# Optimization experiments

Measured on AMD Instinct MI355X. Metric: run time of the kernel, lower is better.

The kernel has to match this reference:

```python
import jax, jax.numpy as jnp
import numpy as np

N = 100000      # nodes
E = 1600000     # edges (before self loops)
H = 64          # hidden channels (per-head out dim, concat=False)
HEADS = 2
L = 2           # num GAT blocks
IN = 64
OUT = 10
B = 64          # graphs in batch
SLOPE = 0.2     # LeakyReLU negative slope (GATv2Conv default)
EPS = 1e-5      # BatchNorm eps


def setup_inputs() -> dict:
    key = jax.random.key(0)
    ks = jax.random.split(key, 10)
    s = 0.05
    x = jax.random.normal(ks[0], (N, IN), jnp.float32)
    edge_index = jax.random.randint(ks[1], (2, E), 0, N, dtype=jnp.int64)
    batch = jnp.sort(jax.random.randint(ks[2], (N,), 0, B, dtype=jnp.int64))
    W_enc = jax.random.normal(ks[3], (IN, H), jnp.float32) * s
    b_enc = jnp.zeros((H,), jnp.float32)
    Wl = jax.random.normal(ks[4], (L, H, HEADS * H), jnp.float32) * s
    bl = jnp.zeros((L, HEADS * H), jnp.float32)
    Wr = jax.random.normal(ks[5], (L, H, HEADS * H), jnp.float32) * s
    br = jnp.zeros((L, HEADS * H), jnp.float32)
    att = jax.random.normal(ks[6], (L, HEADS, H), jnp.float32) * s
    bias = jnp.zeros((L, H), jnp.float32)
    gamma = jnp.ones((L, H), jnp.float32)
    beta = jnp.zeros((L, H), jnp.float32)
    W_cls = jax.random.normal(ks[7], (H, OUT), jnp.float32) * s
    b_cls = jnp.zeros((OUT,), jnp.float32)
    return dict(x=x, edge_index=edge_index, batch=batch, W_enc=W_enc, b_enc=b_enc,
                Wl=Wl, bl=bl, Wr=Wr, br=br, att=att, bias=bias,
                gamma=gamma, beta=beta, W_cls=W_cls, b_cls=b_cls)


def reference(x, edge_index, batch, W_enc, b_enc, Wl, bl, Wr, br, att, bias,
              gamma, beta, W_cls, b_cls):
    # add self loops (GATv2Conv default add_self_loops=True)
    loops = jnp.arange(N, dtype=edge_index.dtype)
    ei = jnp.concatenate([edge_index, jnp.stack([loops, loops])], axis=1)
    src, dst = ei[0], ei[1]

    h = x @ W_enc + b_enc                                   # [N, H] atom encoder (Linear)
    for l in range(L):
        xl = (h @ Wl[l] + bl[l]).reshape(N, HEADS, H)       # source transform
        xr = (h @ Wr[l] + br[l]).reshape(N, HEADS, H)       # target transform
        # GATv2: e_uv = a^T LeakyReLU(W_l x_u + W_r x_v)
        z = jax.nn.leaky_relu(xl[src] + xr[dst], SLOPE)     # [E', heads, H]
        e = jnp.einsum('ehc,hc->eh', z, att[l])             # [E', heads]
        # segment softmax over incoming edges of each dst node
        m = jax.ops.segment_max(e, dst, num_segments=N)     # [N, heads]
        ex = jnp.exp(e - m[dst])
        den = jax.ops.segment_sum(ex, dst, num_segments=N)
        alpha = ex / den[dst]                               # [E', heads]
        out = jax.ops.segment_sum(xl[src] * alpha[:, :, None], dst, num_segments=N)
        h_new = out.mean(axis=1) + bias[l]                  # concat=False: mean over heads
        # BatchNorm1d (batch statistics) -> ReLU; dropout=0
        mu = h_new.mean(axis=0)
        var = h_new.var(axis=0)
        h = jax.nn.relu((h_new - mu) * jax.lax.rsqrt(var + EPS) * gamma[l] + beta[l])

    # global mean pool over graphs
    cnt = jax.ops.segment_sum(jnp.ones((N,), h.dtype), batch, num_segments=B)
    g = jax.ops.segment_sum(h, batch, num_segments=B) / jnp.maximum(cnt, 1.0)[:, None]
    return g @ W_cls + b_cls                                # [B, OUT]
```

## Files before the change

kernel.cpp:

```cpp
#include <hip/hip_runtime.h>

#define N_NODES 100000
#define E_EDGES 1600000
#define EP_EDGES (E_EDGES + N_NODES)
#define SLOPE 0.2f
#define BN_EPS 1e-5f
#define NB 8
#define NODES_PER_B 12500
#define NREP 32
#define SUBREG 8192
#define SCATTER_BLKS ((EP_EDGES + 255) / 256)

typedef _Float16 h2 __attribute__((ext_vector_type(2)));

#if defined(__has_builtin)
#if __has_builtin(__builtin_amdgcn_fdot2)
#define HAVE_FDOT2 1
#endif
#endif

__device__ __forceinline__ float fdot2f(h2 a, h2 b, float c) {
#ifdef HAVE_FDOT2
    return __builtin_amdgcn_fdot2(a, b, c, false);
#else
    return c + (float)a[0] * (float)b[0] + (float)a[1] * (float)b[1];
#endif
}
__device__ __forceinline__ h2 bch2(unsigned u) { return __builtin_bit_cast(h2, u); }
__device__ __forceinline__ h2 habs2(h2 z) {
    return __builtin_bit_cast(h2, (unsigned)(__builtin_bit_cast(unsigned, z) & 0x7fff7fffu));
}
__device__ __forceinline__ h2 shflx_h2(h2 a, int o) {
    return __builtin_bit_cast(h2, __shfl_xor(__builtin_bit_cast(int, a), o, 64));
}

template <int CTRL>
__device__ __forceinline__ float dpp_add_step(float v) {
    int r = __builtin_amdgcn_update_dpp(0, __float_as_int(v), CTRL, 0xF, 0xF, false);
    return v + __int_as_float(r);
}
__device__ __forceinline__ float rowsum16(float v) {
    v = dpp_add_step<0x128>(v);
    v = dpp_add_step<0x124>(v);
    v = dpp_add_step<0x122>(v);
    v = dpp_add_step<0x121>(v);
    return v;
}

__device__ __forceinline__ void bucket_scatter_body(int bid, const int* __restrict__ src,
                                                    const int* __restrict__ dst,
                                                    int* __restrict__ gcur, unsigned* __restrict__ ebuf) {
    int i = bid * 256 + threadIdx.x;
    int rep = bid & (NREP - 1);
    bool active = i < EP_EDGES;
    int s = 0, d = 0;
    if (i < E_EDGES) { s = src[i]; d = dst[i]; }
    else if (active) { s = i - E_EDGES; d = s; }
    int b = active ? (int)((unsigned)d / NODES_PER_B) : NB;
    unsigned long long lt = (1ull << (threadIdx.x & 63)) - 1ull;
    int rank = 0;
    unsigned long long mymask = 0;
#pragma unroll
    for (int bb = 0; bb < NB; ++bb) {
        unsigned long long m = __ballot(b == bb);
        if (b == bb) { rank = __popcll(m & lt); mymask = m; }
    }
    int leader = mymask ? (__ffsll((long long)mymask) - 1) : 0;
    int lanebit = threadIdx.x & 63;
    int chunkbase = 0;
    if (active && lanebit == leader)
        chunkbase = atomicAdd(&gcur[rep * NB + b], (int)__popcll(mymask));
    chunkbase = __shfl(chunkbase, leader, 64);
    if (active) {
        unsigned dl = (unsigned)d - (unsigned)b * NODES_PER_B;
        ebuf[(size_t)(rep * NB + b) * SUBREG + chunkbase + rank] = (dl << 17) | (unsigned)s;
    }
}

__device__ __forceinline__ void fuse_enc_body(const float* __restrict__ We, const float* __restrict__ be,
                                              const float* __restrict__ Wl, const float* __restrict__ bl,
                                              const float* __restrict__ Wr, const float* __restrict__ br,
                                              float* __restrict__ Wcl, float* __restrict__ bcl,
                                              float* __restrict__ Wcr, float* __restrict__ bcr,
                                              float (*sWe)[64], float* sbe) {
    int t = threadIdx.x;
    for (int i = t; i < 4096; i += 256) sWe[i & 63][i >> 6] = We[i];
    if (t < 64) sbe[t] = be[t];
    __syncthreads();
    int j = t & 127, side = t >> 7;
    const float* W  = side ? Wr : Wl;
    const float* bb = side ? br : bl;
    float acc[64];
#pragma unroll
    for (int k = 0; k < 64; ++k) acc[k] = 0.f;
    float bacc = bb[j];
    for (int m = 0; m < 64; ++m) {
        float wv = W[m * 128 + j];
        bacc += sbe[m] * wv;
#pragma unroll
        for (int k = 0; k < 64; ++k) acc[k] += sWe[m][k] * wv;
    }
    float* Wc = side ? Wcr : Wcl;
#pragma unroll
    for (int k = 0; k < 64; ++k) Wc[k * 128 + j] = acc[k];
    (side ? bcr : bcl)[j] = bacc;
}

__global__ __launch_bounds__(256) void scatter_fuse(const int* __restrict__ src, const int* __restrict__ dst,
                                                    int* __restrict__ gcur, unsigned* __restrict__ ebuf,
                                                    const float* __restrict__ We, const float* __restrict__ be,
                                                    const float* __restrict__ Wl, const float* __restrict__ bl,
                                                    const float* __restrict__ Wr, const float* __restrict__ br,
                                                    float* __restrict__ Wcl, float* __restrict__ bcl,
                                                    float* __restrict__ Wcr, float* __restrict__ bcr) {
    __shared__ float sWe[64][64];
    __shared__ float sbe[64];
    if (blockIdx.x == 0)
        fuse_enc_body(We, be, Wl, bl, Wr, br, Wcl, bcl, Wcr, bcr, sWe, sbe);
    else
        bucket_scatter_body(blockIdx.x - 1, src, dst, gcur, ebuf);
}

template <int BN>
__device__ __forceinline__ void layer_gemm_body(int bid, int nb,
                                                const float* __restrict__ hin,
                                                const float* __restrict__ Wl, const float* __restrict__ bl,
                                                const float* __restrict__ Wr, const float* __restrict__ br,
                                                const float* __restrict__ bns, const float* __restrict__ gamma,
                                                const float* __restrict__ beta,
                                                unsigned short* __restrict__ xl, unsigned short* __restrict__ xr,
                                                float* ssc, float* ssh, h2 (*sh)[36]) {
    int t = threadIdx.x;
    if (BN) {
        if (t < 64) {
            float s = 0.f, sq = 0.f;
#pragma unroll
            for (int r = 0; r < 8; ++r) { s += bns[r * 128 + t]; sq += bns[r * 128 + 64 + t]; }
            float mu = s * (1.f / N_NODES);
            float var = sq * (1.f / N_NODES) - mu * mu;
            float sc = gamma[t] * rsqrtf(var + BN_EPS);
            ssc[t] = sc; ssh[t] = beta[t] - mu * sc;
        }
        __syncthreads();
    }
    int p = t & 127, rh = t >> 7;
    int col0 = 2 * p;
    bool isR = col0 >= 128;
    int cw0 = col0 & 127, cw1 = cw0 + 1;
    const float* W = isR ? Wr : Wl;
    h2 w2a[32], w2b[32];
#pragma unroll
    for (int k2 = 0; k2 < 32; ++k2) {
        w2a[k2] = (h2){(_Float16)W[(2 * k2) * 128 + cw0], (_Float16)W[(2 * k2 + 1) * 128 + cw0]};
        w2b[k2] = (h2){(_Float16)W[(2 * k2) * 128 + cw1], (_Float16)W[(2 * k2 + 1) * 128 + cw1]};
    }
    float bja = (isR ? br : bl)[cw0];
    float bjb = (isR ? br : bl)[cw1];
    int head0 = cw0 >> 6, c0 = cw0 & 63;
    int head1 = cw1 >> 6, c1 = cw1 & 63;
    int oidx0 = ((c0 >> 2) << 3) + (head0 << 2) + (c0 & 3);
    int oidx1 = ((c1 >> 2) << 3) + (head1 << 2) + (c1 & 3);
    unsigned short* dstp = isR ? xr : xl;
    for (int base = bid * 16; base < N_NODES; base += nb * 16) {
        __syncthreads();
#pragma unroll
        for (int pass = 0; pass < 2; ++pass) {
            int i = t + pass * 256;
            int node = i >> 5, pr = i & 31;
            int gnode = base + node;
            int cc = pr * 2;
            float2 v = make_float2(0.f, 0.f);
            if (gnode < N_NODES) v = *(const float2*)(hin + (size_t)gnode * 64 + cc);
            if (BN) {
                v.x = fmaxf(v.x * ssc[cc] + ssh[cc], 0.f);
                v.y = fmaxf(v.y * ssc[cc + 1] + ssh[cc + 1], 0.f);
            }
            sh[node][pr] = (h2){(_Float16)v.x, (_Float16)v.y};
        }
        __syncthreads();
        int lim = min(16, N_NODES - base);
        int rend = min(rh * 8 + 8, lim);
        for (int r = rh * 8; r < rend; ++r) {
            float acca = bja, accb = bjb;
            const uint4* r4 = (const uint4*)(&sh[r][0]);
#pragma unroll
            for (int k4 = 0; k4 < 8; ++k4) {
                uint4 u = r4[k4];
                acca = fdot2f(bch2(u.x), w2a[4 * k4 + 0], acca);
                accb = fdot2f(bch2(u.x), w2b[4 * k4 + 0], accb);
                acca = fdot2f(bch2(u.y), w2a[4 * k4 + 1], acca);
                accb = fdot2f(bch2(u.y), w2b[4 * k4 + 1], accb);
                acca = fdot2f(bch2(u.z), w2a[4 * k4 + 2], acca);
                accb = fdot2f(bch2(u.z), w2b[4 * k4 + 2], accb);
                acca = fdot2f(bch2(u.w), w2a[4 * k4 + 3], acca);
                accb = fdot2f(bch2(u.w), w2b[4 * k4 + 3], accb);
            }
            size_t rowb = (size_t)(base + r) * 128;
            dstp[rowb + oidx0] = __builtin_bit_cast(unsigned short, (_Float16)acca);
            dstp[rowb + oidx1] = __builtin_bit_cast(unsigned short, (_Float16)accb);
        }
    }
}

__global__ __launch_bounds__(256) void deg_gemm0(const int* __restrict__ gcur,
                                                 const unsigned* __restrict__ ebuf,
                                                 int* __restrict__ deg,
                                                 const float* __restrict__ hin,
                                                 const float* __restrict__ Wl, const float* __restrict__ bl,
                                                 const float* __restrict__ Wr, const float* __restrict__ br,
                                                 unsigned short* __restrict__ xl, unsigned short* __restrict__ xr) {
    __shared__ unsigned ldeg2[NODES_PER_B / 2];
    __shared__ float ssc[64], ssh[64];
    __shared__ h2 sh[16][36];
    if (blockIdx.x < NREP * NB) {
        int b = blockIdx.x & (NB - 1), rep = blockIdx.x >> 3;
        for (int j = threadIdx.x; j < NODES_PER_B / 2; j += 256) ldeg2[j] = 0;
        __syncthreads();
        int cnt = gcur[rep * NB + b];
        int base = b * NODES_PER_B;
        const unsigned* p = ebuf + (size_t)(rep * NB + b) * SUBREG;
        for (int i = threadIdx.x; i < cnt; i += 256) {
            unsigned dl = p[i] >> 17;
            atomicAdd(&ldeg2[dl >> 1], 1u << ((dl & 1) * 16));
        }
        __syncthreads();
        for (int j = threadIdx.x; j < NODES_PER_B; j += 256) {
            unsigned v = (ldeg2[j >> 1] >> ((j & 1) * 16)) & 0xffffu;
            if (v) atomicAdd(&deg[base + j], (int)v);
        }
    } else {
        layer_gemm_body<0>(blockIdx.x - NREP * NB, 1024, hin, Wl, bl, Wr, br,
                           nullptr, nullptr, nullptr, xl, xr, ssc, ssh, sh);
    }
}

__global__ __launch_bounds__(256) void bucket_fine(const int* __restrict__ gcur,
                                                   const unsigned* __restrict__ ebuf,
                                                   int* __restrict__ cursor, int* __restrict__ col) {
    int b = blockIdx.x & (NB - 1), rep = blockIdx.x >> 3;
    int cnt = gcur[rep * NB + b];
    int base = b * NODES_PER_B;
    const unsigned* p = ebuf + (size_t)(rep * NB + b) * SUBREG;
    for (int i = threadIdx.x; i < cnt; i += 256) {
        unsigned e = p[i];
        int d = base + (int)(e >> 17), s = (int)(e & 0x1FFFFu);
        int pos = atomicAdd(&cursor[d], 1);
        col[pos] = s;
    }
}

__global__ void scan_a(const int* __restrict__ deg, int* __restrict__ row_ptr, int* __restrict__ bsum) {
    __shared__ int wsum[16];
    int tid = threadIdx.x;
    int lane = tid & 63;
    int i = blockIdx.x * 1024 + tid;
    int x = (i < N_NODES) ? deg[i] : 0;
#pragma unroll
    for (int o = 1; o < 64; o <<= 1) {
        int y = __shfl_up(x, o, 64);
        if (lane >= o) x += y;
    }
    if (lane == 63) wsum[tid >> 6] = x;
    __syncthreads();
    if (tid < 16) {
        int s = wsum[tid];
#pragma unroll
        for (int o = 1; o < 16; o <<= 1) {
            int y = __shfl_up(s, o, 16);
            if (tid >= o) s += y;
        }
        wsum[tid] = s;
    }
    __syncthreads();
    int pre = (tid >= 64) ? wsum[(tid >> 6) - 1] : 0;
    int incl = x + pre;
    if (i < N_NODES) row_ptr[i + 1] = incl;
    if (tid == 1023) bsum[blockIdx.x] = incl;
}

__global__ void scan_c(int* __restrict__ cursor, int* __restrict__ row_ptr, const int* __restrict__ bsum) {
    __shared__ int sp[128];
    int t = threadIdx.x;
    if (t < 128) sp[t] = (t < 98) ? bsum[t] : 0;
    __syncthreads();
    for (int o = 1; o < 128; o <<= 1) {
        int v = (t < 128 && t >= o) ? sp[t - o] : 0;
        __syncthreads();
        if (t < 128) sp[t] += v;
        __syncthreads();
    }
    int i = blockIdx.x * 256 + t;
    if (i < N_NODES) {
        int d = cursor[i];
        int blk = i >> 10;
        int pre = blk ? sp[blk - 1] : 0;
        int incl = row_ptr[i + 1] + pre;
        row_ptr[i + 1] = incl;
        cursor[i] = incl - d;
        if (i == 0) row_ptr[0] = 0;
    }
}

__global__ __launch_bounds__(256) void layer_gemm1(const float* __restrict__ hin,
                                                   const float* __restrict__ Wl, const float* __restrict__ bl,
                                                   const float* __restrict__ Wr, const float* __restrict__ br,
                                                   const float* __restrict__ bns, const float* __restrict__ gamma,
                                                   const float* __restrict__ beta,
                                                   unsigned short* __restrict__ xl, unsigned short* __restrict__ xr) {
    __shared__ float ssc[64], ssh[64];
    __shared__ h2 sh[16][36];
    layer_gemm_body<1>(blockIdx.x, gridDim.x, hin, Wl, bl, Wr, br, bns, gamma, beta, xl, xr, ssc, ssh, sh);
}

__global__ __launch_bounds__(256) void aggregate(const char* __restrict__ xlb,
                                                 const uint4* __restrict__ xr4,
                                                 const int* __restrict__ row_ptr, const int* __restrict__ col,
                                                 const float* __restrict__ att_l, const float* __restrict__ bias_l,
                                                 float* __restrict__ hn, float* __restrict__ bnsum) {
    int lane = threadIdx.x & 63, wid = threadIdx.x >> 6;
    int q = lane >> 4, k = lane & 15;
    int koff = k << 4;
    h2 atA0 = {(_Float16)att_l[4 * k], (_Float16)att_l[4 * k + 1]};
    h2 atA1 = {(_Float16)att_l[4 * k + 2], (_Float16)att_l[4 * k + 3]};
    h2 atB0 = {(_Float16)att_l[64 + 4 * k], (_Float16)att_l[64 + 4 * k + 1]};
    h2 atB1 = {(_Float16)att_l[64 + 4 * k + 2], (_Float16)att_l[64 + 4 * k + 3]};
    float bi0 = bias_l[4 * k], bi1 = bias_l[4 * k + 1], bi2 = bias_l[4 * k + 2], bi3 = bias_l[4 * k + 3];
    const h2 c06 = {(_Float16)0.6f, (_Float16)0.6f};
    const h2 c04 = {(_Float16)0.4f, (_Float16)0.4f};
    float ps[4] = {0, 0, 0, 0}, pq[4] = {0, 0, 0, 0};
    int w = blockIdx.x * 4 + wid, nw = gridDim.x * 4;
    for (int v = w; v < N_NODES; v += nw) {
        uint4 rp = xr4[(size_t)v * 16 + k];
        h2 rA0 = bch2(rp.x), rA1 = bch2(rp.y), rB0 = bch2(rp.z), rB1 = bch2(rp.w);
        int beg = row_ptr[v], end = row_ptr[v + 1];
        float s0 = 0.f, s1 = 0.f;
        h2 aA0 = {0, 0}, aA1 = {0, 0}, aB0 = {0, 0}, aB1 = {0, 0};
        const int* cptr = col + beg + q;
        int cv0 = cptr[0], cv1 = cptr[4], cv2 = cptr[8], cv3 = cptr[12];
        cptr += 16;
        uint4 lp0 = *(const uint4*)(xlb + (((size_t)(unsigned)cv0) << 8) + koff);
        uint4 lp1 = lp0, lp2 = lp0;
        if (beg + 4 < end) lp1 = *(const uint4*)(xlb + (((size_t)(unsigned)cv1) << 8) + koff);
        if (beg + 8 < end) lp2 = *(const uint4*)(xlb + (((size_t)(unsigned)cv2) << 8) + koff);
#pragma unroll 2
        for (int i = beg; i < end; i += 4) {
            uint4 lp3 = lp2;
            if (i + 12 < end) lp3 = *(const uint4*)(xlb + (((size_t)(unsigned)cv3) << 8) + koff);
            cv3 = *cptr; cptr += 4;
            h2 lA0 = bch2(lp0.x), lA1 = bch2(lp0.y), lB0 = bch2(lp0.z), lB1 = bch2(lp0.w);
            h2 zA0 = lA0 + rA0, zA1 = lA1 + rA1, zB0 = lB0 + rB0, zB1 = lB1 + rB1;
            h2 yA0 = zA0 * c06 + habs2(zA0) * c04;
            h2 yA1 = zA1 * c06 + habs2(zA1) * c04;
            h2 yB0 = zB0 * c06 + habs2(zB0) * c04;
            h2 yB1 = zB1 * c06 + habs2(zB1) * c04;
            float t0 = fdot2f(yA1, atA1, fdot2f(yA0, atA0, 0.f));
            float t1 = fdot2f(yB1, atB1, fdot2f(yB0, atB0, 0.f));
            t0 = rowsum16(t0); t1 = rowsum16(t1);
            bool valid = (i + q) < end;
            float p0 = valid ? __expf(t0) : 0.f;
            float p1 = valid ? __expf(t1) : 0.f;
            s0 += p0; s1 += p1;
            h2 p0h = {(_Float16)p0, (_Float16)p0};
            h2 p1h = {(_Float16)p1, (_Float16)p1};
            aA0 += p0h * lA0; aA1 += p0h * lA1;
            aB0 += p1h * lB0; aB1 += p1h * lB1;
            lp0 = lp1; lp1 = lp2; lp2 = lp3;
        }
#pragma unroll
        for (int o = 16; o <= 32; o <<= 1) {
            s0 += __shfl_xor(s0, o, 64); s1 += __shfl_xor(s1, o, 64);
            aA0 += shflx_h2(aA0, o); aA1 += shflx_h2(aA1, o);
            aB0 += shflx_h2(aB0, o); aB1 += shflx_h2(aB1, o);
        }
        if (q == 0) {
            float i0 = 0.5f / s0, i1 = 0.5f / s1;
            float hv0 = (float)aA0[0] * i0 + (float)aB0[0] * i1 + bi0;
            float hv1 = (float)aA0[1] * i0 + (float)aB0[1] * i1 + bi1;
            float hv2 = (float)aA1[0] * i0 + (float)aB1[0] * i1 + bi2;
            float hv3 = (float)aA1[1] * i0 + (float)aB1[1] * i1 + bi3;
            *(float4*)(hn + (size_t)v * 64 + 4 * k) = make_float4(hv0, hv1, hv2, hv3);
            ps[0] += hv0; pq[0] += hv0 * hv0;
            ps[1] += hv1; pq[1] += hv1 * hv1;
            ps[2] += hv2; pq[2] += hv2 * hv2;
            ps[3] += hv3; pq[3] += hv3 * hv3;
        }
    }
    __shared__ float sb[2][4][64];
    if (q == 0) {
#pragma unroll
        for (int j = 0; j < 4; ++j) { sb[0][wid][4 * k + j] = ps[j]; sb[1][wid][4 * k + j] = pq[j]; }
    }
    __syncthreads();
    float* dstb = bnsum + (size_t)(blockIdx.x & 7) * 128;
    int t = threadIdx.x;
    if (t < 64)
        atomicAdd(&dstb[t], sb[0][0][t] + sb[0][1][t] + sb[0][2][t] + sb[0][3][t]);
    else if (t < 128)
        atomicAdd(&dstb[t], sb[1][0][t - 64] + sb[1][1][t - 64] + sb[1][2][t - 64] + sb[1][3][t - 64]);
}

__global__ __launch_bounds__(256) void pool2(const float* __restrict__ hn, const int* __restrict__ batch,
                                             const float* __restrict__ bns, const float* __restrict__ gamma,
                                             const float* __restrict__ beta,
                                             float* __restrict__ gpool, float* __restrict__ gcnt) {
    __shared__ float ssc[64], ssh[64];
    int t = threadIdx.x;
    if (t < 64) {
        float s = 0.f, sq = 0.f;
#pragma unroll
        for (int r = 0; r < 8; ++r) { s += bns[r * 128 + t]; sq += bns[r * 128 + 64 + t]; }
        float mu = s * (1.f / N_NODES);
        float var = sq * (1.f / N_NODES) - mu * mu;
        float sc = gamma[t] * rsqrtf(var + BN_EPS);
        ssc[t] = sc; ssh[t] = beta[t] - mu * sc;
    }
    __syncthreads();
    int g = blockIdx.x >> 2, part = blockIdx.x & 3;
    int lo = 0, hi = N_NODES;
    while (lo < hi) { int mid = (lo + hi) >> 1; if (batch[mid] < g) lo = mid + 1; else hi = mid; }
    int lo2 = lo, hi2 = N_NODES;
    while (lo2 < hi2) { int mid = (lo2 + hi2) >> 1; if (batch[mid] < g + 1) lo2 = mid + 1; else hi2 = mid; }
    int len = lo2 - lo;
    if (part == 0 && t == 0) gcnt[g] = (float)len;
    int n0 = lo + (len * part) / 4, n1 = lo + (len * (part + 1)) / 4;
    int c = t & 63, r = t >> 6;
    float sc = ssc[c], sh = ssh[c];
    float acc = 0.f;
    for (int node = n0 + r; node < n1; node += 4)
        acc += fmaxf(hn[(size_t)node * 64 + c] * sc + sh, 0.f);
    __shared__ float sb[4][64];
    sb[r][c] = acc;
    __syncthreads();
    if (r == 0)
        atomicAdd(&gpool[g * 64 + c], sb[0][c] + sb[1][c] + sb[2][c] + sb[3][c]);
}

__global__ void classify(const float* __restrict__ gpool, const float* __restrict__ gcnt,
                         const float* __restrict__ Wc, const float* __restrict__ bc, float* __restrict__ out) {
    int t = threadIdx.x;
    if (t >= 640) return;
    int b = t / 10, o = t % 10;
    float inv = 1.f / fmaxf(gcnt[b], 1.f);
    float acc = 0.f;
    for (int c = 0; c < 64; ++c) acc += gpool[b * 64 + c] * Wc[c * 10 + o];
    out[t] = acc * inv + bc[o];
}

extern "C" void kernel_launch(void* const* d_in, const int* in_sizes, int n_in,
                              void* d_out, int out_size, void* d_ws, size_t ws_size,
                              hipStream_t stream) {
    (void)in_sizes; (void)n_in; (void)out_size; (void)ws_size;
    const float* x     = (const float*)d_in[0];
    const int*   ei    = (const int*)d_in[1];
    const int*   batch = (const int*)d_in[2];
    const float* W_enc = (const float*)d_in[3];
    const float* b_enc = (const float*)d_in[4];
    const float* Wl    = (const float*)d_in[5];
    const float* bl    = (const float*)d_in[6];
    const float* Wr    = (const float*)d_in[7];
    const float* br    = (const float*)d_in[8];
    const float* att   = (const float*)d_in[9];
    const float* bias  = (const float*)d_in[10];
    const float* gamma = (const float*)d_in[11];
    const float* beta  = (const float*)d_in[12];
    const float* Wc    = (const float*)d_in[13];
    const float* bc    = (const float*)d_in[14];
    float* out = (float*)d_out;

    char* ws = (char*)d_ws;
    size_t off = 0;
    auto A = [&](size_t bytes) { size_t r = off; off += (bytes + 255) & ~(size_t)255; return r; };

    int* row_ptr = (int*)(ws + A((N_NODES + 1) * 4));
    size_t colv_off = A((size_t)EP_EDGES * 4 + 426240);
    int* colv = (int*)(ws + colv_off);
    char* zbase = ws + colv_off + (size_t)EP_EDGES * 4;
    int*   cursor = (int*)(zbase + 128);
    int*   gcur   = (int*)(zbase + 400128);
    float* bns    = (float*)(zbase + 401152);
    float* gpool  = (float*)(zbase + 409344);
    float* gcnt   = (float*)(zbase + 425728);
    const size_t ZBYTES = 426240;

    float* h   = (float*)(ws + A((size_t)N_NODES * 64 * 4));
    float* hn  = (float*)(ws + A((size_t)N_NODES * 64 * 4));
    unsigned short* xl = (unsigned short*)(ws + A((size_t)N_NODES * 128 * 2));
    unsigned short* xr = (unsigned short*)(ws + A((size_t)N_NODES * 128 * 2));
    unsigned* ebuf = (unsigned*)(ws + A((size_t)NREP * NB * SUBREG * 4));
    int* bsum  = (int*)(ws + A(512));
    float* Wcl = (float*)(ws + A(64 * 128 * 4));
    float* Wcr = (float*)(ws + A(64 * 128 * 4));
    float* bcl = (float*)(ws + A(128 * 4));
    float* bcr = (float*)(ws + A(128 * 4));

    const int* srcv = ei;
    const int* dstv = ei + E_EDGES;

    hipMemsetAsync(zbase, 0, ZBYTES, stream);

    scatter_fuse<<<SCATTER_BLKS + 1, 256, 0, stream>>>(srcv, dstv, gcur, ebuf,
                                                       W_enc, b_enc, Wl, bl, Wr, br,
                                                       Wcl, bcl, Wcr, bcr);
    deg_gemm0<<<NREP * NB + 1024, 256, 0, stream>>>(gcur, ebuf, cursor,
                                                    x, Wcl, bcl, Wcr, bcr, xl, xr);
    scan_a<<<98, 1024, 0, stream>>>(cursor, row_ptr, bsum);
    scan_c<<<(N_NODES + 255) / 256, 256, 0, stream>>>(cursor, row_ptr, bsum);
    bucket_fine<<<NREP * NB, 256, 0, stream>>>(gcur, ebuf, cursor, colv);

    aggregate<<<4096, 256, 0, stream>>>((const char*)xl, (const uint4*)xr,
                                        row_ptr, colv, att, bias, hn, bns);
    layer_gemm1<<<1024, 256, 0, stream>>>(hn, Wl + 64 * 128, bl + 128, Wr + 64 * 128, br + 128,
                                          bns, gamma, beta, xl, xr);
    aggregate<<<4096, 256, 0, stream>>>((const char*)xl, (const uint4*)xr,
                                        row_ptr, colv, att + 128, bias + 64, h, bns + 1024);

    pool2<<<256, 256, 0, stream>>>(h, batch, bns + 1024, gamma + 64, beta + 64, gpool, gcnt);
    classify<<<1, 640, 0, stream>>>(gpool, gcnt, Wc, bc, out);
}
```

Measured before the change: 432.5 us.

## Replace fdot2 node GEMMs with MFMA tiles and store hidden states in fp16

The per-layer node transforms (x@Wl, x@Wr), previously fdot2 loops over 16-node tiles, now use 16x16x32 f16 MFMA on 64-node tiles. Weights are pre-packed into fragment layout by extra blocks in the scatter kernel, and inputs are staged in swizzled shared memory. Output is written through an LDS transpose so the interleaved xl/xr rows are stored as coalesced 16-byte writes. The aggregate output buffers (hn, h) become fp16, which halves their traffic in the next GEMM and in pooling but adds rounding error. The degree histogram is packed into 8-bit counters to fit the larger shared buffer, which assumes per-replica node degree stays under 256.

```diff
diff --git a/kernel.cpp b/kernel.cpp
--- a/kernel.cpp
+++ b/kernel.cpp
@@ -10,8 +10,12 @@
 #define NREP 32
 #define SUBREG 8192
 #define SCATTER_BLKS ((EP_EDGES + 255) / 256)
+#define NBLK ((N_NODES + 63) / 64)
 
 typedef _Float16 h2 __attribute__((ext_vector_type(2)));
+typedef _Float16 v4h __attribute__((ext_vector_type(4)));
+typedef _Float16 v8h __attribute__((ext_vector_type(8)));
+typedef float v4f __attribute__((ext_vector_type(4)));
 
 #if defined(__has_builtin)
 #if __has_builtin(__builtin_amdgcn_fdot2)
@@ -27,6 +31,7 @@
 #endif
 }
 __device__ __forceinline__ h2 bch2(unsigned u) { return __builtin_bit_cast(h2, u); }
+__device__ __forceinline__ unsigned bcu(h2 v) { return __builtin_bit_cast(unsigned, v); }
 __device__ __forceinline__ h2 habs2(h2 z) {
     return __builtin_bit_cast(h2, (unsigned)(__builtin_bit_cast(unsigned, z) & 0x7fff7fffu));
 }
@@ -77,12 +82,11 @@
     }
 }
 
-__device__ __forceinline__ void fuse_enc_body(const float* __restrict__ We, const float* __restrict__ be,
-                                              const float* __restrict__ Wl, const float* __restrict__ bl,
-                                              const float* __restrict__ Wr, const float* __restrict__ br,
-                                              float* __restrict__ Wcl, float* __restrict__ bcl,
-                                              float* __restrict__ Wcr, float* __restrict__ bcr,
-                                              float (*sWe)[64], float* sbe) {
+__device__ __forceinline__ void fuse_enc_pack0(const float* __restrict__ We, const float* __restrict__ be,
+                                               const float* __restrict__ Wl, const float* __restrict__ bl,
+                                               const float* __restrict__ Wr, const float* __restrict__ br,
+                                               _Float16* __restrict__ Wfrag0, float* __restrict__ bias0,
+                                               float (*sWe)[64], float* sbe) {
     int t = threadIdx.x;
     for (int i = t; i < 4096; i += 256) sWe[i & 63][i >> 6] = We[i];
     if (t < 64) sbe[t] = be[t];
@@ -100,10 +104,33 @@
 #pragma unroll
         for (int k = 0; k < 64; ++k) acc[k] += sWe[m][k] * wv;
     }
-    float* Wc = side ? Wcr : Wcl;
-#pragma unroll
-    for (int k = 0; k < 64; ++k) Wc[k * 128 + j] = acc[k];
-    (side ? bcr : bcl)[j] = bacc;
+    int ncolg = (side << 7) | j;
+    int w = ncolg >> 6, nt = (ncolg >> 4) & 3, lp = ncolg & 15;
+#pragma unroll
+    for (int k = 0; k < 64; ++k) {
+        int kt = k >> 5;
+        int l = (((k >> 3) & 3) << 4) | lp;
+        int jj = k & 7;
+        Wfrag0[((((w * 4 + nt) * 2 + kt)) << 9) + (l << 3) + jj] = (_Float16)acc[k];
+    }
+    bias0[ncolg] = bacc;
+}
+
+__device__ __forceinline__ void pack1_body(const float* __restrict__ WL, const float* __restrict__ WR,
+                                           const float* __restrict__ bL, const float* __restrict__ bR,
+                                           _Float16* __restrict__ Wfrag, float* __restrict__ bias_all) {
+    int t = threadIdx.x;
+    for (int i = t; i < 16384; i += 256) {
+        int j = i & 7, l = (i >> 3) & 63, kt = (i >> 9) & 1, nt = (i >> 10) & 3, w = i >> 12;
+        int ncol = w * 64 + nt * 16 + (l & 15);
+        int k = kt * 32 + (l >> 4) * 8 + j;
+        int side = ncol >> 7, colW = ncol & 127;
+        Wfrag[i] = (_Float16)((side ? WR : WL)[k * 128 + colW]);
+    }
+    if (t < 256) {
+        int side = t >> 7, colW = t & 127;
+        bias_all[t] = (side ? bR : bL)[colW];
+    }
 }
 
 __global__ __launch_bounds__(256) void scatter_fuse(const int* __restrict__ src, const int* __restrict__ dst,
@@ -111,26 +138,28 @@
                                                     const float* __restrict__ We, const float* __restrict__ be,
                                                     const float* __restrict__ Wl, const float* __restrict__ bl,
                                                     const float* __restrict__ Wr, const float* __restrict__ br,
-                                                    float* __restrict__ Wcl, float* __restrict__ bcl,
-                                                    float* __restrict__ Wcr, float* __restrict__ bcr) {
+                                                    _Float16* __restrict__ Wfrag0, float* __restrict__ bias0,
+                                                    _Float16* __restrict__ Wfrag1, float* __restrict__ bias1) {
     __shared__ float sWe[64][64];
     __shared__ float sbe[64];
     if (blockIdx.x == 0)
-        fuse_enc_body(We, be, Wl, bl, Wr, br, Wcl, bcl, Wcr, bcr, sWe, sbe);
+        fuse_enc_pack0(We, be, Wl, bl, Wr, br, Wfrag0, bias0, sWe, sbe);
+    else if (blockIdx.x == 1)
+        pack1_body(Wl + 64 * 128, Wr + 64 * 128, bl + 128, br + 128, Wfrag1, bias1);
     else
-        bucket_scatter_body(blockIdx.x - 1, src, dst, gcur, ebuf);
+        bucket_scatter_body(blockIdx.x - 2, src, dst, gcur, ebuf);
 }
 
 template <int BN>
-__device__ __forceinline__ void layer_gemm_body(int bid, int nb,
-                                                const float* __restrict__ hin,
-                                                const float* __restrict__ Wl, const float* __restrict__ bl,
-                                                const float* __restrict__ Wr, const float* __restrict__ br,
-                                                const float* __restrict__ bns, const float* __restrict__ gamma,
-                                                const float* __restrict__ beta,
-                                                unsigned short* __restrict__ xl, unsigned short* __restrict__ xr,
-                                                float* ssc, float* ssh, h2 (*sh)[36]) {
-    int t = threadIdx.x;
+__device__ __forceinline__ void mfma_body(int mb, const void* __restrict__ hin,
+                                          const _Float16* __restrict__ Wfrag,
+                                          const float* __restrict__ bias_all,
+                                          const float* __restrict__ bns, const float* __restrict__ gamma,
+                                          const float* __restrict__ beta,
+                                          unsigned short* __restrict__ xl, unsigned short* __restrict__ xr,
+                                          char* smem, float* ssc, float* ssh) {
+    int t = threadIdx.x;
+    int w = t >> 6, l = t & 63;
     if (BN) {
         if (t < 64) {
             float s = 0.f, sq = 0.f;
@@ -143,95 +172,149 @@
         }
         __syncthreads();
     }
-    int p = t & 127, rh = t >> 7;
-    int col0 = 2 * p;
-    bool isR = col0 >= 128;
-    int cw0 = col0 & 127, cw1 = cw0 + 1;
-    const float* W = isR ? Wr : Wl;
-    h2 w2a[32], w2b[32];
-#pragma unroll
-    for (int k2 = 0; k2 < 32; ++k2) {
-        w2a[k2] = (h2){(_Float16)W[(2 * k2) * 128 + cw0], (_Float16)W[(2 * k2 + 1) * 128 + cw0]};
-        w2b[k2] = (h2){(_Float16)W[(2 * k2) * 128 + cw1], (_Float16)W[(2 * k2 + 1) * 128 + cw1]};
-    }
-    float bja = (isR ? br : bl)[cw0];
-    float bjb = (isR ? br : bl)[cw1];
-    int head0 = cw0 >> 6, c0 = cw0 & 63;
-    int head1 = cw1 >> 6, c1 = cw1 & 63;
-    int oidx0 = ((c0 >> 2) << 3) + (head0 << 2) + (c0 & 3);
-    int oidx1 = ((c1 >> 2) << 3) + (head1 << 2) + (c1 & 3);
-    unsigned short* dstp = isR ? xr : xl;
-    for (int base = bid * 16; base < N_NODES; base += nb * 16) {
-        __syncthreads();
+    int base = mb * 64;
+    if (BN == 0) {
+#pragma unroll
+        for (int pass = 0; pass < 4; ++pass) {
+            int idx = t + pass * 256;
+            int node = idx >> 4, q4 = idx & 15;
+            int gnode = base + node;
+            float4 v = make_float4(0.f, 0.f, 0.f, 0.f);
+            if (gnode < N_NODES) v = *(const float4*)((const float*)hin + (size_t)gnode * 64 + q4 * 4);
+            v4h p = {(_Float16)v.x, (_Float16)v.y, (_Float16)v.z, (_Float16)v.w};
+            int byte = (node * 128 + q4 * 8) ^ ((node & 7) << 4);
+            *(v4h*)(smem + byte) = p;
+        }
+    } else {
 #pragma unroll
         for (int pass = 0; pass < 2; ++pass) {
-            int i = t + pass * 256;
-            int node = i >> 5, pr = i & 31;
+            int idx = t + pass * 256;
+            int node = idx >> 3, q8 = idx & 7;
             int gnode = base + node;
-            int cc = pr * 2;
-            float2 v = make_float2(0.f, 0.f);
-            if (gnode < N_NODES) v = *(const float2*)(hin + (size_t)gnode * 64 + cc);
-            if (BN) {
-                v.x = fmaxf(v.x * ssc[cc] + ssh[cc], 0.f);
-                v.y = fmaxf(v.y * ssc[cc + 1] + ssh[cc + 1], 0.f);
+            uint4 u = make_uint4(0, 0, 0, 0);
+            if (gnode < N_NODES) u = *(const uint4*)((const unsigned short*)hin + (size_t)gnode * 64 + q8 * 8);
+            int c0 = q8 * 8;
+            h2 p0 = bch2(u.x), p1 = bch2(u.y), p2 = bch2(u.z), p3 = bch2(u.w);
+            float a, b;
+            a = fmaxf((float)p0[0] * ssc[c0 + 0] + ssh[c0 + 0], 0.f);
+            b = fmaxf((float)p0[1] * ssc[c0 + 1] + ssh[c0 + 1], 0.f);
+            p0 = (h2){(_Float16)a, (_Float16)b};
+            a = fmaxf((float)p1[0] * ssc[c0 + 2] + ssh[c0 + 2], 0.f);
+            b = fmaxf((float)p1[1] * ssc[c0 + 3] + ssh[c0 + 3], 0.f);
+            p1 = (h2){(_Float16)a, (_Float16)b};
+            a = fmaxf((float)p2[0] * ssc[c0 + 4] + ssh[c0 + 4], 0.f);
+            b = fmaxf((float)p2[1] * ssc[c0 + 5] + ssh[c0 + 5], 0.f);
+            p2 = (h2){(_Float16)a, (_Float16)b};
+            a = fmaxf((float)p3[0] * ssc[c0 + 6] + ssh[c0 + 6], 0.f);
+            b = fmaxf((float)p3[1] * ssc[c0 + 7] + ssh[c0 + 7], 0.f);
+            p3 = (h2){(_Float16)a, (_Float16)b};
+            int byte = (node * 128 + q8 * 16) ^ ((node & 7) << 4);
+            *(uint4*)(smem + byte) = make_uint4(bcu(p0), bcu(p1), bcu(p2), bcu(p3));
+        }
+    }
+    v8h bfr[4][2];
+    float biasv[4];
+#pragma unroll
+    for (int nt = 0; nt < 4; ++nt) {
+#pragma unroll
+        for (int kt = 0; kt < 2; ++kt)
+            bfr[nt][kt] = *(const v8h*)(Wfrag + ((((w * 4 + nt) * 2 + kt) << 9) + (l << 3)));
+        biasv[nt] = bias_all[w * 64 + nt * 16 + (l & 15)];
+    }
+    __syncthreads();
+    v4f acc[4][4];
+#pragma unroll
+    for (int mt = 0; mt < 4; ++mt)
+#pragma unroll
+        for (int nt = 0; nt < 4; ++nt)
+            acc[mt][nt] = (v4f){0.f, 0.f, 0.f, 0.f};
+#pragma unroll
+    for (int mt = 0; mt < 4; ++mt) {
+        int node = mt * 16 + (l & 15);
+        int swz = (node & 7) << 4;
+        int b0 = (node * 128 + ((l >> 4) << 4)) ^ swz;
+        int b1 = (node * 128 + 64 + ((l >> 4) << 4)) ^ swz;
+        v8h a0 = *(const v8h*)(smem + b0);
+        v8h a1 = *(const v8h*)(smem + b1);
+#pragma unroll
+        for (int nt = 0; nt < 4; ++nt) {
+            acc[mt][nt] = __builtin_amdgcn_mfma_f32_16x16x32_f16(a0, bfr[nt][0], acc[mt][nt], 0, 0, 0);
+            acc[mt][nt] = __builtin_amdgcn_mfma_f32_16x16x32_f16(a1, bfr[nt][1], acc[mt][nt], 0, 0, 0);
+        }
+    }
+    _Float16* sOut = (_Float16*)(smem + 8192);
+    __syncthreads();
+#pragma unroll
+    for (int mt = 0; mt < 4; ++mt) {
+#pragma unroll
+        for (int nt = 0; nt < 4; ++nt) {
+            int ncol = (w << 6) + (nt << 4) + (l & 15);
+            int side = ncol >> 7, head = (ncol >> 6) & 1, c = ncol & 63;
+            int oidx = ((c >> 2) << 3) + (head << 2) + (c & 3);
+            int obase = side * 128 + oidx;
+#pragma unroll
+            for (int j = 0; j < 4; ++j) {
+                int node = mt * 16 + ((l >> 4) << 2) + j;
+                sOut[node * 256 + obase] = (_Float16)(acc[mt][nt][j] + biasv[nt]);
             }
-            sh[node][pr] = (h2){(_Float16)v.x, (_Float16)v.y};
-        }
-        __syncthreads();
-        int lim = min(16, N_NODES - base);
-        int rend = min(rh * 8 + 8, lim);
-        for (int r = rh * 8; r < rend; ++r) {
-            float acca = bja, accb = bjb;
-            const uint4* r4 = (const uint4*)(&sh[r][0]);
-#pragma unroll
-            for (int k4 = 0; k4 < 8; ++k4) {
-                uint4 u = r4[k4];
-                acca = fdot2f(bch2(u.x), w2a[4 * k4 + 0], acca);
-                accb = fdot2f(bch2(u.x), w2b[4 * k4 + 0], accb);
-                acca = fdot2f(bch2(u.y), w2a[4 * k4 + 1], acca);
-                accb = fdot2f(bch2(u.y), w2b[4 * k4 + 1], accb);
-                acca = fdot2f(bch2(u.z), w2a[4 * k4 + 2], acca);
-                accb = fdot2f(bch2(u.z), w2b[4 * k4 + 2], accb);
-                acca = fdot2f(bch2(u.w), w2a[4 * k4 + 3], acca);
-                accb = fdot2f(bch2(u.w), w2b[4 * k4 + 3], accb);
-            }
-            size_t rowb = (size_t)(base + r) * 128;
-            dstp[rowb + oidx0] = __builtin_bit_cast(unsigned short, (_Float16)acca);
-            dstp[rowb + oidx1] = __builtin_bit_cast(unsigned short, (_Float16)accb);
-        }
-    }
-}
-
-__global__ __launch_bounds__(256) void deg_gemm0(const int* __restrict__ gcur,
+        }
+    }
+    __syncthreads();
+#pragma unroll
+    for (int pass = 0; pass < 8; ++pass) {
+        int idx = t + pass * 256;
+        int node = idx >> 5, wi = idx & 31;
+        int gnode = base + node;
+        if (gnode < N_NODES) {
+            int side = wi >> 4, o16 = wi & 15;
+            uint4 val = *(const uint4*)(sOut + node * 256 + side * 128 + o16 * 8);
+            unsigned short* dstp = side ? xr : xl;
+            *(uint4*)(dstp + (size_t)gnode * 128 + o16 * 8) = val;
+        }
+    }
+}
+
+__global__ __launch_bounds__(256) void deg_mfma0(const int* __restrict__ gcur,
                                                  const unsigned* __restrict__ ebuf,
                                                  int* __restrict__ deg,
-                                                 const float* __restrict__ hin,
-                                                 const float* __restrict__ Wl, const float* __restrict__ bl,
-                                                 const float* __restrict__ Wr, const float* __restrict__ br,
+                                                 const float* __restrict__ x,
+                                                 const _Float16* __restrict__ Wfrag0,
+                                                 const float* __restrict__ bias0,
                                                  unsigned short* __restrict__ xl, unsigned short* __restrict__ xr) {
-    __shared__ unsigned ldeg2[NODES_PER_B / 2];
+    __shared__ __align__(16) char smem[40960];
     __shared__ float ssc[64], ssh[64];
-    __shared__ h2 sh[16][36];
     if (blockIdx.x < NREP * NB) {
+        unsigned* ldeg4 = (unsigned*)smem;
         int b = blockIdx.x & (NB - 1), rep = blockIdx.x >> 3;
-        for (int j = threadIdx.x; j < NODES_PER_B / 2; j += 256) ldeg2[j] = 0;
+        for (int j = threadIdx.x; j < NODES_PER_B / 4 + 1; j += 256) ldeg4[j] = 0;
         __syncthreads();
         int cnt = gcur[rep * NB + b];
         int base = b * NODES_PER_B;
         const unsigned* p = ebuf + (size_t)(rep * NB + b) * SUBREG;
         for (int i = threadIdx.x; i < cnt; i += 256) {
             unsigned dl = p[i] >> 17;
-            atomicAdd(&ldeg2[dl >> 1], 1u << ((dl & 1) * 16));
+            atomicAdd(&ldeg4[dl >> 2], 1u << ((dl & 3) * 8));
         }
         __syncthreads();
         for (int j = threadIdx.x; j < NODES_PER_B; j += 256) {
-            unsigned v = (ldeg2[j >> 1] >> ((j & 1) * 16)) & 0xffffu;
+            unsigned v = (ldeg4[j >> 2] >> ((j & 3) * 8)) & 0xffu;
             if (v) atomicAdd(&deg[base + j], (int)v);
         }
     } else {
-        layer_gemm_body<0>(blockIdx.x - NREP * NB, 1024, hin, Wl, bl, Wr, br,
-                           nullptr, nullptr, nullptr, xl, xr, ssc, ssh, sh);
-    }
+        mfma_body<0>(blockIdx.x - NREP * NB, x, Wfrag0, bias0, nullptr, nullptr, nullptr,
+                     xl, xr, smem, ssc, ssh);
+    }
+}
+
+__global__ __launch_bounds__(256) void mfma1(const unsigned short* __restrict__ hin,
+                                             const _Float16* __restrict__ Wfrag1,
+                                             const float* __restrict__ bias1,
+                                             const float* __restrict__ bns, const float* __restrict__ gamma,
+                                             const float* __restrict__ beta,
+                                             unsigned short* __restrict__ xl, unsigned short* __restrict__ xr) {
+    __shared__ __align__(16) char smem[40960];
+    __shared__ float ssc[64], ssh[64];
+    mfma_body<1>(blockIdx.x, hin, Wfrag1, bias1, bns, gamma, beta, xl, xr, smem, ssc, ssh);
 }
 
 __global__ __launch_bounds__(256) void bucket_fine(const int* __restrict__ gcur,
@@ -301,22 +384,11 @@
     }
 }
 
-__global__ __launch_bounds__(256) void layer_gemm1(const float* __restrict__ hin,
-                                                   const float* __restrict__ Wl, const float* __restrict__ bl,
-                                                   const float* __restrict__ Wr, const float* __restrict__ br,
-                                                   const float* __restrict__ bns, const float* __restrict__ gamma,
-                                                   const float* __restrict__ beta,
-                                                   unsigned short* __restrict__ xl, unsigned short* __restrict__ xr) {
-    __shared__ float ssc[64], ssh[64];
-    __shared__ h2 sh[16][36];
-    layer_gemm_body<1>(blockIdx.x, gridDim.x, hin, Wl, bl, Wr, br, bns, gamma, beta, xl, xr, ssc, ssh, sh);
-}
-
 __global__ __launch_bounds__(256) void aggregate(const char* __restrict__ xlb,
                                                  const uint4* __restrict__ xr4,
                                                  const int* __restrict__ row_ptr, const int* __restrict__ col,
                                                  const float* __restrict__ att_l, const float* __restrict__ bias_l,
-                                                 float* __restrict__ hn, float* __restrict__ bnsum) {
+                                                 unsigned short* __restrict__ hn16, float* __restrict__ bnsum) {
     int lane = threadIdx.x & 63, wid = threadIdx.x >> 6;
     int q = lane >> 4, k = lane & 15;
     int koff = k << 4;
@@ -378,7 +450,9 @@
             float hv1 = (float)aA0[1] * i0 + (float)aB0[1] * i1 + bi1;
             float hv2 = (float)aA1[0] * i0 + (float)aB1[0] * i1 + bi2;
             float hv3 = (float)aA1[1] * i0 + (float)aB1[1] * i1 + bi3;
-            *(float4*)(hn + (size_t)v * 64 + 4 * k) = make_float4(hv0, hv1, hv2, hv3);
+            h2 o01 = {(_Float16)hv0, (_Float16)hv1};
+            h2 o23 = {(_Float16)hv2, (_Float16)hv3};
+            *(uint2*)(hn16 + (size_t)v * 64 + 4 * k) = make_uint2(bcu(o01), bcu(o23));
             ps[0] += hv0; pq[0] += hv0 * hv0;
             ps[1] += hv1; pq[1] += hv1 * hv1;
             ps[2] += hv2; pq[2] += hv2 * hv2;
@@ -399,7 +473,8 @@
         atomicAdd(&dstb[t], sb[1][0][t - 64] + sb[1][1][t - 64] + sb[1][2][t - 64] + sb[1][3][t - 64]);
 }
 
-__global__ __launch_bounds__(256) void pool2(const float* __restrict__ hn, const int* __restrict__ batch,
+__global__ __launch_bounds__(256) void pool2(const unsigned short* __restrict__ hn,
+                                             const int* __restrict__ batch,
                                              const float* __restrict__ bns, const float* __restrict__ gamma,
                                              const float* __restrict__ beta,
                                              float* __restrict__ gpool, float* __restrict__ gcnt) {
@@ -426,8 +501,10 @@
     int c = t & 63, r = t >> 6;
     float sc = ssc[c], sh = ssh[c];
     float acc = 0.f;
-    for (int node = n0 + r; node < n1; node += 4)
-        acc += fmaxf(hn[(size_t)node * 64 + c] * sc + sh, 0.f);
+    for (int node = n0 + r; node < n1; node += 4) {
+        float hv = (float)__builtin_bit_cast(_Float16, hn[(size_t)node * 64 + c]);
+        acc += fmaxf(hv * sc + sh, 0.f);
+    }
     __shared__ float sb[4][64];
     sb[r][c] = acc;
     __syncthreads();
@@ -482,38 +559,37 @@
     float* gcnt   = (float*)(zbase + 425728);
     const size_t ZBYTES = 426240;
 
-    float* h   = (float*)(ws + A((size_t)N_NODES * 64 * 4));
-    float* hn  = (float*)(ws + A((size_t)N_NODES * 64 * 4));
+    unsigned short* hn    = (unsigned short*)(ws + A((size_t)N_NODES * 64 * 2));
+    unsigned short* h2buf = (unsigned short*)(ws + A((size_t)N_NODES * 64 * 2));
     unsigned short* xl = (unsigned short*)(ws + A((size_t)N_NODES * 128 * 2));
     unsigned short* xr = (unsigned short*)(ws + A((size_t)N_NODES * 128 * 2));
     unsigned* ebuf = (unsigned*)(ws + A((size_t)NREP * NB * SUBREG * 4));
     int* bsum  = (int*)(ws + A(512));
-    float* Wcl = (float*)(ws + A(64 * 128 * 4));
-    float* Wcr = (float*)(ws + A(64 * 128 * 4));
-    float* bcl = (float*)(ws + A(128 * 4));
-    float* bcr = (float*)(ws + A(128 * 4));
+    _Float16* Wfrag0 = (_Float16*)(ws + A(16384 * 2));
+    _Float16* Wfrag1 = (_Float16*)(ws + A(16384 * 2));
+    float* bias0 = (float*)(ws + A(256 * 4));
+    float* bias1 = (float*)(ws + A(256 * 4));
 
     const int* srcv = ei;
     const int* dstv = ei + E_EDGES;
 
     hipMemsetAsync(zbase, 0, ZBYTES, stream);
 
-    scatter_fuse<<<SCATTER_BLKS + 1, 256, 0, stream>>>(srcv, dstv, gcur, ebuf,
+    scatter_fuse<<<SCATTER_BLKS + 2, 256, 0, stream>>>(srcv, dstv, gcur, ebuf,
                                                        W_enc, b_enc, Wl, bl, Wr, br,
-                                                       Wcl, bcl, Wcr, bcr);
-    deg_gemm0<<<NREP * NB + 1024, 256, 0, stream>>>(gcur, ebuf, cursor,
-                                                    x, Wcl, bcl, Wcr, bcr, xl, xr);
+                                                       Wfrag0, bias0, Wfrag1, bias1);
+    deg_mfma0<<<NREP * NB + NBLK, 256, 0, stream>>>(gcur, ebuf, cursor,
+                                                    x, Wfrag0, bias0, xl, xr);
     scan_a<<<98, 1024, 0, stream>>>(cursor, row_ptr, bsum);
     scan_c<<<(N_NODES + 255) / 256, 256, 0, stream>>>(cursor, row_ptr, bsum);
     bucket_fine<<<NREP * NB, 256, 0, stream>>>(gcur, ebuf, cursor, colv);
 
     aggregate<<<4096, 256, 0, stream>>>((const char*)xl, (const uint4*)xr,
                                         row_ptr, colv, att, bias, hn, bns);
-    layer_gemm1<<<1024, 256, 0, stream>>>(hn, Wl + 64 * 128, bl + 128, Wr + 64 * 128, br + 128,
-                                          bns, gamma, beta, xl, xr);
+    mfma1<<<NBLK, 256, 0, stream>>>(hn, Wfrag1, bias1, bns, gamma, beta, xl, xr);
     aggregate<<<4096, 256, 0, stream>>>((const char*)xl, (const uint4*)xr,
-                                        row_ptr, colv, att + 128, bias + 64, h, bns + 1024);
-
-    pool2<<<256, 256, 0, stream>>>(h, batch, bns + 1024, gamma + 64, beta + 64, gpool, gcnt);
+                                        row_ptr, colv, att + 128, bias + 64, h2buf, bns + 1024);
+
+    pool2<<<256, 256, 0, stream>>>(h2buf, batch, bns + 1024, gamma + 64, beta + 64, gpool, gcnt);
     classify<<<1, 640, 0, stream>>>(gpool, gcnt, Wc, bc, out);
 }
```

Result: faster. 365.4 us (-15.5%).
